# Kernel optimization log

Hardware: AMD Instinct MI355X
Metric: run time of the kernel (lower is better)

Reference implementation:

```python
import jax, jax.numpy as jnp
import numpy as np

N_NODES = 100000
N_EDGES = 1600000
LN_EPS = 1e-5
CLAMP = 1.8


def setup_inputs() -> dict:
    key = jax.random.key(0)
    ks = jax.random.split(key, 12)
    feats = [100, 64, 64, 47]
    inp = {
        "x": jax.random.normal(ks[0], (N_NODES, feats[0]), dtype=jnp.float32),
        "adj_vals": jax.random.uniform(ks[1], (N_EDGES,), dtype=jnp.float32),
        "adj_row": jax.random.randint(ks[2], (N_EDGES,), 0, N_NODES),
        "adj_col": jax.random.randint(ks[3], (N_EDGES,), 0, N_NODES),
        "ln_gamma": jnp.ones((feats[0],), dtype=jnp.float32),
        "ln_beta": jnp.zeros((feats[0],), dtype=jnp.float32),
    }
    for i in range(3):
        fi, fo = feats[i], feats[i + 1]
        bound = 1.0 / np.sqrt(fi)
        inp[f"W{i+1}"] = jax.random.uniform(ks[4 + 2 * i], (fi, fo), minval=-bound, maxval=bound, dtype=jnp.float32)
        inp[f"b{i+1}"] = jax.random.uniform(ks[5 + 2 * i], (fo,), minval=-bound, maxval=bound, dtype=jnp.float32)
    return inp


def _spmm(vals, row, col, x):
    # out[i] = sum_{e: row[e]==i} vals[e] * x[col[e]]
    gathered = vals[:, None] * x[col]  # [E, D]
    return jax.ops.segment_sum(gathered, row, num_segments=N_NODES)


def reference(x, adj_vals, adj_row, adj_col, ln_gamma, ln_beta, W1, b1, W2, b2, W3, b3):
    # clamp to [-1.8, 1.8]: relu(x+1.8)-1.8 then 1.8-relu(1.8-x)
    x = jnp.clip(x, -CLAMP, CLAMP)
    # LayerNorm over last dim (100)
    mu = jnp.mean(x, axis=-1, keepdims=True)
    var = jnp.mean(jnp.square(x - mu), axis=-1, keepdims=True)
    x = (x - mu) * jax.lax.rsqrt(var + LN_EPS) * ln_gamma + ln_beta
    # GCN layers: Linear -> spmm -> (elu except last); dropout=0 => identity
    x = jax.nn.elu(_spmm(adj_vals, adj_row, adj_col, x @ W1 + b1))
    x = jax.nn.elu(_spmm(adj_vals, adj_row, adj_col, x @ W2 + b2))
    x = _spmm(adj_vals, adj_row, adj_col, x @ W3 + b3)
    return x
```

## Files before the change

kernel.cpp:

```cpp
#include <hip/hip_runtime.h>
#include <cstdint>
#include <cstddef>

#define N_NODES_C 100000
#define N_EDGES_C 1600000
#define LN_EPS_C 1e-5f
#define CLAMP_C 1.8f
#define SC_BLOCKS 1024
#define LN_BLOCKS 1024

typedef unsigned short ushort_t;

__device__ __forceinline__ float readlane_f(float v, int l) {
  return __uint_as_float(__builtin_amdgcn_readlane(__float_as_uint(v), l));
}

__device__ __forceinline__ float wave_sum(float v) {
#pragma unroll
  for (int off = 32; off > 0; off >>= 1) v += __shfl_xor(v, off, 64);
  return v;
}

__device__ __forceinline__ ushort_t f2bf(float f) {
  unsigned u = __float_as_uint(f);
  unsigned r = (u + 0x7fffu + ((u >> 16) & 1u)) >> 16;
  return (ushort_t)r;
}
__device__ __forceinline__ float bf2f(ushort_t u) {
  return __uint_as_float((unsigned)u << 16);
}

__global__ void hist_kernel(const int* __restrict__ row, int* __restrict__ counts) {
  int stride = gridDim.x * blockDim.x;
  for (int e = blockIdx.x * blockDim.x + threadIdx.x; e < N_EDGES_C; e += stride)
    atomicAdd(&counts[row[e]], 1);
}

__global__ void scan1_kernel(const int* __restrict__ counts, int* __restrict__ rowstart,
                             int* __restrict__ bsums) {
  __shared__ int lds[256];
  int t = threadIdx.x;
  int base = blockIdx.x * 1024 + t * 4;
  int c0 = (base + 0 < N_NODES_C) ? counts[base + 0] : 0;
  int c1 = (base + 1 < N_NODES_C) ? counts[base + 1] : 0;
  int c2 = (base + 2 < N_NODES_C) ? counts[base + 2] : 0;
  int c3 = (base + 3 < N_NODES_C) ? counts[base + 3] : 0;
  int s = c0 + c1 + c2 + c3;
  lds[t] = s;
  __syncthreads();
#pragma unroll
  for (int off = 1; off < 256; off <<= 1) {
    int v = (t >= off) ? lds[t - off] : 0;
    __syncthreads();
    lds[t] += v;
    __syncthreads();
  }
  int incl = lds[t];
  int excl = incl - s;
  if (t == 255) bsums[blockIdx.x] = incl;
  if (base + 0 < N_NODES_C) rowstart[base + 0] = excl;
  excl += c0;
  if (base + 1 < N_NODES_C) rowstart[base + 1] = excl;
  excl += c1;
  if (base + 2 < N_NODES_C) rowstart[base + 2] = excl;
  excl += c2;
  if (base + 3 < N_NODES_C) rowstart[base + 3] = excl;
}

__global__ void scan2_kernel(int* __restrict__ bsums, int nb) {
  __shared__ int lds[128];
  int t = threadIdx.x;
  int v = (t < nb) ? bsums[t] : 0;
  lds[t] = v;
  __syncthreads();
#pragma unroll
  for (int off = 1; off < 128; off <<= 1) {
    int u = (t >= off) ? lds[t - off] : 0;
    __syncthreads();
    lds[t] += u;
    __syncthreads();
  }
  if (t < nb) bsums[t] = lds[t] - v;
}

__global__ void scan3_kernel(int* __restrict__ rowstart, int* __restrict__ cursor,
                             const int* __restrict__ bsums) {
  int add = bsums[blockIdx.x];
  int base = blockIdx.x * 1024 + threadIdx.x * 4;
#pragma unroll
  for (int i = 0; i < 4; ++i)
    if (base + i < N_NODES_C) {
      int v = rowstart[base + i] + add;
      rowstart[base + i] = v;
      cursor[base + i] = v;
    }
}

__global__ __launch_bounds__(256) void scatter_ln_kernel(
    const int* __restrict__ row, const int* __restrict__ col,
    const float* __restrict__ vals, int* __restrict__ cursor,
    int2* __restrict__ edges_s,
    const float* __restrict__ x, const float* __restrict__ gamma,
    const float* __restrict__ beta, const float* __restrict__ W1,
    const float* __restrict__ b1, ushort_t* __restrict__ y) {
  if ((blockIdx.x & 1) == 0) {
    int tid = (blockIdx.x >> 1) * 256 + threadIdx.x;
    const int nt = SC_BLOCKS * 256;
    int r[8], c[8], p[8];
    float v[8];
#pragma unroll
    for (int k = 0; k < 8; ++k) {
      int e = tid + k * nt;
      bool in = e < N_EDGES_C;
      r[k] = in ? row[e] : 0;
      c[k] = in ? col[e] : 0;
      v[k] = in ? vals[e] : 0.f;
    }
#pragma unroll
    for (int k = 0; k < 8; ++k) {
      int e = tid + k * nt;
      if (e < N_EDGES_C) p[k] = atomicAdd(&cursor[r[k]], 1);
    }
#pragma unroll
    for (int k = 0; k < 8; ++k) {
      int e = tid + k * nt;
      if (e < N_EDGES_C) edges_s[p[k]] = make_int2(c[k], __float_as_int(v[k]));
    }
  } else {
    int lane = threadIdx.x & 63;
    int wid = (blockIdx.x >> 1) * 4 + (threadIdx.x >> 6);
    const int nw = LN_BLOCKS * 4;
    float bias = b1[lane];
    float g0 = gamma[lane];
    float be0 = beta[lane];
    float g1 = (lane < 36) ? gamma[64 + lane] : 0.f;
    float be1 = (lane < 36) ? beta[64 + lane] : 0.f;
    for (int n = wid; n < N_NODES_C; n += nw) {
      const float* xr = x + (size_t)n * 100;
      float x0 = xr[lane];
      float x1 = (lane < 36) ? xr[64 + lane] : 0.f;
      x0 = fminf(fmaxf(x0, -CLAMP_C), CLAMP_C);
      x1 = fminf(fmaxf(x1, -CLAMP_C), CLAMP_C);
      float mu = wave_sum(x0 + x1) * 0.01f;
      float d0 = x0 - mu;
      float d1 = (lane < 36) ? (x1 - mu) : 0.f;
      float var = wave_sum(d0 * d0 + d1 * d1) * 0.01f;
      float inv = rsqrtf(var + LN_EPS_C);
      float xn0 = d0 * inv * g0 + be0;
      float xn1 = d1 * inv * g1 + be1;
      float acc = bias;
#pragma unroll
      for (int k = 0; k < 64; ++k) acc = fmaf(readlane_f(xn0, k), W1[k * 64 + lane], acc);
#pragma unroll
      for (int k = 0; k < 36; ++k) acc = fmaf(readlane_f(xn1, k), W1[(64 + k) * 64 + lane], acc);
      y[(size_t)n * 64 + lane] = f2bf(acc);
    }
  }
}

template <int DOUT>
__global__ __launch_bounds__(256) void spmm_elu_gemm_kernel(
    const int* __restrict__ rowstart, const int* __restrict__ counts,
    const int2* __restrict__ edges_s, const ushort_t* __restrict__ yb,
    const float* __restrict__ W, const float* __restrict__ b,
    ushort_t* __restrict__ out) {
  int lane = threadIdx.x & 63;
  int wid = blockIdx.x * (blockDim.x >> 6) + (threadIdx.x >> 6);
  int nw = gridDim.x * (blockDim.x >> 6);
  float w[64];
#pragma unroll
  for (int k = 0; k < 64; ++k) w[k] = (lane < DOUT) ? W[k * DOUT + lane] : 0.f;
  float bias = (lane < DOUT) ? b[lane] : 0.f;
  for (int n = wid; n < N_NODES_C; n += nw) {
    int start = rowstart[n];
    int cnt = counts[n];
    float a[8];
#pragma unroll
    for (int u = 0; u < 8; ++u) a[u] = 0.f;
    for (int base = 0; base < cnt; base += 64) {
      int m = cnt - base;
      if (m > 64) m = 64;
      int2 ev = make_int2(0, 0);
      if (lane < m) ev = edges_s[start + base + lane];
      int mr = (m + 15) & ~15;
      for (int j = 0; j < mr; j += 16) {
        float g[16];
#pragma unroll
        for (int u = 0; u < 16; ++u)
          g[u] = bf2f(yb[(size_t)__builtin_amdgcn_readlane(ev.x, j + u) * 64 + lane]);
#pragma unroll
        for (int u = 0; u < 16; ++u)
          a[u & 7] = fmaf(
              __uint_as_float(__builtin_amdgcn_readlane((unsigned)ev.y, j + u)), g[u],
              a[u & 7]);
      }
    }
    float acc = ((a[0] + a[1]) + (a[2] + a[3])) + ((a[4] + a[5]) + (a[6] + a[7]));
    float xe = (acc > 0.f) ? acc : expm1f(acc);
    float o = bias;
#pragma unroll
    for (int k = 0; k < 64; ++k) o = fmaf(readlane_f(xe, k), w[k], o);
    if (lane < DOUT) out[(size_t)n * 64 + lane] = f2bf(o);
  }
}

__global__ __launch_bounds__(256) void spmm_final_kernel(
    const int* __restrict__ rowstart, const int* __restrict__ counts,
    const int2* __restrict__ edges_s, const ushort_t* __restrict__ yb,
    float* __restrict__ out) {
  int lane = threadIdx.x & 63;
  int wid = blockIdx.x * (blockDim.x >> 6) + (threadIdx.x >> 6);
  int nw = gridDim.x * (blockDim.x >> 6);
  int lmask = (lane < 47) ? lane : 46;
  for (int n = wid; n < N_NODES_C; n += nw) {
    int start = rowstart[n];
    int cnt = counts[n];
    float a[8];
#pragma unroll
    for (int u = 0; u < 8; ++u) a[u] = 0.f;
    for (int base = 0; base < cnt; base += 64) {
      int m = cnt - base;
      if (m > 64) m = 64;
      int2 ev = make_int2(0, 0);
      if (lane < m) ev = edges_s[start + base + lane];
      int mr = (m + 15) & ~15;
      for (int j = 0; j < mr; j += 16) {
        float g[16];
#pragma unroll
        for (int u = 0; u < 16; ++u)
          g[u] = bf2f(yb[(size_t)__builtin_amdgcn_readlane(ev.x, j + u) * 64 + lmask]);
#pragma unroll
        for (int u = 0; u < 16; ++u)
          a[u & 7] = fmaf(
              __uint_as_float(__builtin_amdgcn_readlane((unsigned)ev.y, j + u)), g[u],
              a[u & 7]);
      }
    }
    float acc = ((a[0] + a[1]) + (a[2] + a[3])) + ((a[4] + a[5]) + (a[6] + a[7]));
    if (lane < 47) out[(size_t)n * 47 + lane] = acc;
  }
}

extern "C" void kernel_launch(void* const* d_in, const int* in_sizes, int n_in,
                              void* d_out, int out_size, void* d_ws, size_t ws_size,
                              hipStream_t stream) {
  const float* x = (const float*)d_in[0];
  const float* adj_vals = (const float*)d_in[1];
  const int* adj_row = (const int*)d_in[2];
  const int* adj_col = (const int*)d_in[3];
  const float* gamma = (const float*)d_in[4];
  const float* beta = (const float*)d_in[5];
  const float* W1 = (const float*)d_in[6];
  const float* b1 = (const float*)d_in[7];
  const float* W2 = (const float*)d_in[8];
  const float* b2 = (const float*)d_in[9];
  const float* W3 = (const float*)d_in[10];
  const float* b3 = (const float*)d_in[11];
  float* out = (float*)d_out;

  char* ws = (char*)d_ws;
  size_t off = 0;
  auto alloc = [&](size_t bytes) -> void* {
    void* p = ws + off;
    off += (bytes + 255) & ~(size_t)255;
    return p;
  };
  ushort_t* bufA = (ushort_t*)alloc(sizeof(ushort_t) * (size_t)N_NODES_C * 64);
  ushort_t* bufB = (ushort_t*)alloc(sizeof(ushort_t) * (size_t)N_NODES_C * 64);
  int* counts = (int*)alloc(sizeof(int) * N_NODES_C);
  int* cursor = (int*)alloc(sizeof(int) * N_NODES_C);
  int* rowstart = (int*)alloc(sizeof(int) * N_NODES_C);
  int* bsums = (int*)alloc(sizeof(int) * 256);
  int2* edges_s = (int2*)alloc(sizeof(int2) * N_EDGES_C);

  hipMemsetAsync(counts, 0, sizeof(int) * N_NODES_C, stream);

  hist_kernel<<<2048, 256, 0, stream>>>(adj_row, counts);
  int nb = (N_NODES_C + 1023) / 1024;
  scan1_kernel<<<nb, 256, 0, stream>>>(counts, rowstart, bsums);
  scan2_kernel<<<1, 128, 0, stream>>>(bsums, nb);
  scan3_kernel<<<nb, 256, 0, stream>>>(rowstart, cursor, bsums);

  scatter_ln_kernel<<<SC_BLOCKS + LN_BLOCKS, 256, 0, stream>>>(
      adj_row, adj_col, adj_vals, cursor, edges_s, x, gamma, beta, W1, b1, bufA);

  spmm_elu_gemm_kernel<64><<<2048, 256, 0, stream>>>(rowstart, counts, edges_s, bufA,
                                                     W2, b2, bufB);
  spmm_elu_gemm_kernel<47><<<2048, 256, 0, stream>>>(rowstart, counts, edges_s, bufB,
                                                     W3, b3, bufA);
  spmm_final_kernel<<<2048, 256, 0, stream>>>(rowstart, counts, edges_s, bufA, out);
}
```

Measured before the change: 403.4 us.

## Process two nodes per wave in SpMM kernels and batch histogram loads

Each wave now handles two adjacent nodes at once, interleaving their gathers so that more independent memory loads are in flight to hide gather latency. The W matrix is no longer cached in 64 registers; it is reloaded from memory during the output GEMV, which frees registers for the doubled gather buffers. The histogram kernel loads eight row indices per thread before issuing its atomics, using a smaller grid sized to cover all edges in one pass. Risks include register pressure from the doubled buffers, extra load traffic for W, and imbalance when the two paired nodes have different degrees.

Measured after the change: 698.9 us. 73.2% more time.

```diff
diff --git a/kernel.cpp b/kernel.cpp
--- a/kernel.cpp
+++ b/kernel.cpp
@@ -30,10 +30,19 @@
   return __uint_as_float((unsigned)u << 16);
 }
 
-__global__ void hist_kernel(const int* __restrict__ row, int* __restrict__ counts) {
-  int stride = gridDim.x * blockDim.x;
-  for (int e = blockIdx.x * blockDim.x + threadIdx.x; e < N_EDGES_C; e += stride)
-    atomicAdd(&counts[row[e]], 1);
+__global__ __launch_bounds__(256) void hist_kernel(const int* __restrict__ row,
+                                                   int* __restrict__ counts) {
+  int tid = blockIdx.x * blockDim.x + threadIdx.x;
+  int nt = gridDim.x * blockDim.x;
+  int r[8];
+#pragma unroll
+  for (int k = 0; k < 8; ++k) {
+    int e = tid + k * nt;
+    r[k] = (e < N_EDGES_C) ? row[e] : -1;
+  }
+#pragma unroll
+  for (int k = 0; k < 8; ++k)
+    if (r[k] >= 0) atomicAdd(&counts[r[k]], 1);
 }
 
 __global__ void scan1_kernel(const int* __restrict__ counts, int* __restrict__ rowstart,
@@ -165,42 +174,106 @@
     const float* __restrict__ W, const float* __restrict__ b,
     ushort_t* __restrict__ out) {
   int lane = threadIdx.x & 63;
-  int wid = blockIdx.x * (blockDim.x >> 6) + (threadIdx.x >> 6);
-  int nw = gridDim.x * (blockDim.x >> 6);
-  float w[64];
-#pragma unroll
-  for (int k = 0; k < 64; ++k) w[k] = (lane < DOUT) ? W[k * DOUT + lane] : 0.f;
+  int wid = blockIdx.x * 4 + (threadIdx.x >> 6);
+  int nw = gridDim.x * 4;
   float bias = (lane < DOUT) ? b[lane] : 0.f;
-  for (int n = wid; n < N_NODES_C; n += nw) {
-    int start = rowstart[n];
-    int cnt = counts[n];
-    float a[8];
-#pragma unroll
-    for (int u = 0; u < 8; ++u) a[u] = 0.f;
-    for (int base = 0; base < cnt; base += 64) {
-      int m = cnt - base;
+  for (int n0 = 2 * wid; n0 < N_NODES_C; n0 += 2 * nw) {
+    int nA = n0, nB = n0 + 1;
+    bool hasB = nB < N_NODES_C;
+    int sA = rowstart[nA];
+    int cA = counts[nA];
+    int sB = hasB ? rowstart[nB] : 0;
+    int cB = hasB ? counts[nB] : 0;
+    int mA = cA < 64 ? cA : 64;
+    int mB = cB < 64 ? cB : 64;
+    int2 evA = make_int2(0, 0), evB = make_int2(0, 0);
+    if (lane < mA) evA = edges_s[sA + lane];
+    if (lane < mB) evB = edges_s[sB + lane];
+    float aA[4] = {0.f, 0.f, 0.f, 0.f};
+    float aB[4] = {0.f, 0.f, 0.f, 0.f};
+    int mrA = (mA + 15) & ~15;
+    int mrB = (mB + 15) & ~15;
+    int mr = mrA > mrB ? mrA : mrB;
+    for (int j = 0; j < mr; j += 16) {
+      bool doA = j < mrA, doB = j < mrB;
+      float gA[16], gB[16];
+      if (doA) {
+#pragma unroll
+        for (int u = 0; u < 16; ++u)
+          gA[u] = bf2f(yb[(size_t)__builtin_amdgcn_readlane(evA.x, j + u) * 64 + lane]);
+      }
+      if (doB) {
+#pragma unroll
+        for (int u = 0; u < 16; ++u)
+          gB[u] = bf2f(yb[(size_t)__builtin_amdgcn_readlane(evB.x, j + u) * 64 + lane]);
+      }
+      if (doA) {
+#pragma unroll
+        for (int u = 0; u < 16; ++u)
+          aA[u & 3] = fmaf(
+              __uint_as_float(__builtin_amdgcn_readlane((unsigned)evA.y, j + u)), gA[u],
+              aA[u & 3]);
+      }
+      if (doB) {
+#pragma unroll
+        for (int u = 0; u < 16; ++u)
+          aB[u & 3] = fmaf(
+              __uint_as_float(__builtin_amdgcn_readlane((unsigned)evB.y, j + u)), gB[u],
+              aB[u & 3]);
+      }
+    }
+    for (int base = 64; base < cA; base += 64) {
+      int m = cA - base;
       if (m > 64) m = 64;
       int2 ev = make_int2(0, 0);
-      if (lane < m) ev = edges_s[start + base + lane];
-      int mr = (m + 15) & ~15;
-      for (int j = 0; j < mr; j += 16) {
+      if (lane < m) ev = edges_s[sA + base + lane];
+      int mre = (m + 15) & ~15;
+      for (int j = 0; j < mre; j += 16) {
         float g[16];
 #pragma unroll
         for (int u = 0; u < 16; ++u)
           g[u] = bf2f(yb[(size_t)__builtin_amdgcn_readlane(ev.x, j + u) * 64 + lane]);
 #pragma unroll
         for (int u = 0; u < 16; ++u)
-          a[u & 7] = fmaf(
+          aA[u & 3] = fmaf(
               __uint_as_float(__builtin_amdgcn_readlane((unsigned)ev.y, j + u)), g[u],
-              a[u & 7]);
-      }
-    }
-    float acc = ((a[0] + a[1]) + (a[2] + a[3])) + ((a[4] + a[5]) + (a[6] + a[7]));
-    float xe = (acc > 0.f) ? acc : expm1f(acc);
-    float o = bias;
-#pragma unroll
-    for (int k = 0; k < 64; ++k) o = fmaf(readlane_f(xe, k), w[k], o);
-    if (lane < DOUT) out[(size_t)n * 64 + lane] = f2bf(o);
+              aA[u & 3]);
+      }
+    }
+    for (int base = 64; base < cB; base += 64) {
+      int m = cB - base;
+      if (m > 64) m = 64;
+      int2 ev = make_int2(0, 0);
+      if (lane < m) ev = edges_s[sB + base + lane];
+      int mre = (m + 15) & ~15;
+      for (int j = 0; j < mre; j += 16) {
+        float g[16];
+#pragma unroll
+        for (int u = 0; u < 16; ++u)
+          g[u] = bf2f(yb[(size_t)__builtin_amdgcn_readlane(ev.x, j + u) * 64 + lane]);
+#pragma unroll
+        for (int u = 0; u < 16; ++u)
+          aB[u & 3] = fmaf(
+              __uint_as_float(__builtin_amdgcn_readlane((unsigned)ev.y, j + u)), g[u],
+              aB[u & 3]);
+      }
+    }
+    float accA = (aA[0] + aA[1]) + (aA[2] + aA[3]);
+    float xeA = (accA > 0.f) ? accA : expm1f(accA);
+    float oA = bias;
+#pragma unroll
+    for (int k = 0; k < 64; ++k)
+      oA = fmaf(readlane_f(xeA, k), (lane < DOUT) ? W[k * DOUT + lane] : 0.f, oA);
+    if (lane < DOUT) out[(size_t)nA * 64 + lane] = f2bf(oA);
+    if (hasB) {
+      float accB = (aB[0] + aB[1]) + (aB[2] + aB[3]);
+      float xeB = (accB > 0.f) ? accB : expm1f(accB);
+      float oB = bias;
+#pragma unroll
+      for (int k = 0; k < 64; ++k)
+        oB = fmaf(readlane_f(xeB, k), (lane < DOUT) ? W[k * DOUT + lane] : 0.f, oB);
+      if (lane < DOUT) out[(size_t)nB * 64 + lane] = f2bf(oB);
+    }
   }
 }
 
@@ -209,35 +282,96 @@
     const int2* __restrict__ edges_s, const ushort_t* __restrict__ yb,
     float* __restrict__ out) {
   int lane = threadIdx.x & 63;
-  int wid = blockIdx.x * (blockDim.x >> 6) + (threadIdx.x >> 6);
-  int nw = gridDim.x * (blockDim.x >> 6);
+  int wid = blockIdx.x * 4 + (threadIdx.x >> 6);
+  int nw = gridDim.x * 4;
   int lmask = (lane < 47) ? lane : 46;
-  for (int n = wid; n < N_NODES_C; n += nw) {
-    int start = rowstart[n];
-    int cnt = counts[n];
-    float a[8];
-#pragma unroll
-    for (int u = 0; u < 8; ++u) a[u] = 0.f;
-    for (int base = 0; base < cnt; base += 64) {
-      int m = cnt - base;
+  for (int n0 = 2 * wid; n0 < N_NODES_C; n0 += 2 * nw) {
+    int nA = n0, nB = n0 + 1;
+    bool hasB = nB < N_NODES_C;
+    int sA = rowstart[nA];
+    int cA = counts[nA];
+    int sB = hasB ? rowstart[nB] : 0;
+    int cB = hasB ? counts[nB] : 0;
+    int mA = cA < 64 ? cA : 64;
+    int mB = cB < 64 ? cB : 64;
+    int2 evA = make_int2(0, 0), evB = make_int2(0, 0);
+    if (lane < mA) evA = edges_s[sA + lane];
+    if (lane < mB) evB = edges_s[sB + lane];
+    float aA[4] = {0.f, 0.f, 0.f, 0.f};
+    float aB[4] = {0.f, 0.f, 0.f, 0.f};
+    int mrA = (mA + 15) & ~15;
+    int mrB = (mB + 15) & ~15;
+    int mr = mrA > mrB ? mrA : mrB;
+    for (int j = 0; j < mr; j += 16) {
+      bool doA = j < mrA, doB = j < mrB;
+      float gA[16], gB[16];
+      if (doA) {
+#pragma unroll
+        for (int u = 0; u < 16; ++u)
+          gA[u] = bf2f(yb[(size_t)__builtin_amdgcn_readlane(evA.x, j + u) * 64 + lmask]);
+      }
+      if (doB) {
+#pragma unroll
+        for (int u = 0; u < 16; ++u)
+          gB[u] = bf2f(yb[(size_t)__builtin_amdgcn_readlane(evB.x, j + u) * 64 + lmask]);
+      }
+      if (doA) {
+#pragma unroll
+        for (int u = 0; u < 16; ++u)
+          aA[u & 3] = fmaf(
+              __uint_as_float(__builtin_amdgcn_readlane((unsigned)evA.y, j + u)), gA[u],
+              aA[u & 3]);
+      }
+      if (doB) {
+#pragma unroll
+        for (int u = 0; u < 16; ++u)
+          aB[u & 3] = fmaf(
+              __uint_as_float(__builtin_amdgcn_readlane((unsigned)evB.y, j + u)), gB[u],
+              aB[u & 3]);
+      }
+    }
+    for (int base = 64; base < cA; base += 64) {
+      int m = cA - base;
       if (m > 64) m = 64;
       int2 ev = make_int2(0, 0);
-      if (lane < m) ev = edges_s[start + base + lane];
-      int mr = (m + 15) & ~15;
-      for (int j = 0; j < mr; j += 16) {
+      if (lane < m) ev = edges_s[sA + base + lane];
+      int mre = (m + 15) & ~15;
+      for (int j = 0; j < mre; j += 16) {
         float g[16];
 #pragma unroll
         for (int u = 0; u < 16; ++u)
           g[u] = bf2f(yb[(size_t)__builtin_amdgcn_readlane(ev.x, j + u) * 64 + lmask]);
 #pragma unroll
         for (int u = 0; u < 16; ++u)
-          a[u & 7] = fmaf(
+          aA[u & 3] = fmaf(
               __uint_as_float(__builtin_amdgcn_readlane((unsigned)ev.y, j + u)), g[u],
-              a[u & 7]);
-      }
-    }
-    float acc = ((a[0] + a[1]) + (a[2] + a[3])) + ((a[4] + a[5]) + (a[6] + a[7]));
-    if (lane < 47) out[(size_t)n * 47 + lane] = acc;
+              aA[u & 3]);
+      }
+    }
+    for (int base = 64; base < cB; base += 64) {
+      int m = cB - base;
+      if (m > 64) m = 64;
+      int2 ev = make_int2(0, 0);
+      if (lane < m) ev = edges_s[sB + base + lane];
+      int mre = (m + 15) & ~15;
+      for (int j = 0; j < mre; j += 16) {
+        float g[16];
+#pragma unroll
+        for (int u = 0; u < 16; ++u)
+          g[u] = bf2f(yb[(size_t)__builtin_amdgcn_readlane(ev.x, j + u) * 64 + lmask]);
+#pragma unroll
+        for (int u = 0; u < 16; ++u)
+          aB[u & 3] = fmaf(
+              __uint_as_float(__builtin_amdgcn_readlane((unsigned)ev.y, j + u)), g[u],
+              aB[u & 3]);
+      }
+    }
+    float accA = (aA[0] + aA[1]) + (aA[2] + aA[3]);
+    if (lane < 47) out[(size_t)nA * 47 + lane] = accA;
+    if (hasB) {
+      float accB = (aB[0] + aB[1]) + (aB[2] + aB[3]);
+      if (lane < 47) out[(size_t)nB * 47 + lane] = accB;
+    }
   }
 }
 
@@ -275,7 +409,7 @@
 
   hipMemsetAsync(counts, 0, sizeof(int) * N_NODES_C, stream);
 
-  hist_kernel<<<2048, 256, 0, stream>>>(adj_row, counts);
+  hist_kernel<<<782, 256, 0, stream>>>(adj_row, counts);
   int nb = (N_NODES_C + 1023) / 1024;
   scan1_kernel<<<nb, 256, 0, stream>>>(counts, rowstart, bsums);
   scan2_kernel<<<1, 128, 0, stream>>>(bsums, nb);
```
